# Kernel optimization log

Hardware: AMD Instinct MI355X
Metric: run time of the kernel (lower is better)

The kernel has to match this reference:

```python
import jax, jax.numpy as jnp
import numpy as np

LMDA = 1.0
SMOOTH = 1e-05

# 13 directional offsets (dz, dy, dx) matching the original slice pairs 1..13
OFFSETS = [
    (1, 0, 0), (0, 1, 0), (0, 0, 1),
    (1, 1, 0), (1, -1, 0),
    (0, 1, 1), (0, 1, -1),
    (1, 0, -1), (1, 0, 1),
    (1, -1, -1), (1, 1, -1),
    (-1, -1, -1), (-1, 1, -1),
]


def _shifted_diff(x, off):
    """x[..., pos-shift] - x[..., neg-shift] for offset off over last 3 dims."""
    sl_pos = tuple(slice(1, None) if o == 1 else (slice(None, -1) if o == -1 else slice(None)) for o in off)
    sl_neg = tuple(slice(None, -1) if o == 1 else (slice(1, None) if o == -1 else slice(None)) for o in off)
    return x[(Ellipsis,) + sl_pos] - x[(Ellipsis,) + sl_neg]


def setup_inputs() -> dict:
    key = jax.random.key(0)
    k1, k2 = jax.random.split(key)
    shape = (4, 1, 128, 192, 192)
    eps = 1e-6
    inp = jax.random.uniform(k1, shape, dtype=jnp.float32, minval=eps, maxval=1.0 - eps)
    tgt = jax.random.uniform(k2, shape, dtype=jnp.float32, minval=0.0, maxval=1.0)
    return {"input": inp, "target": tgt}


def reference(input, target):
    # region term: BCE with mean reduction
    bce = -jnp.mean(target * jnp.log(input) + (1.0 - target) * jnp.log(1.0 - input))

    # boundary term: 13 directional diff-product ratios
    acc = jnp.float32(0.0)
    for off in OFFSETS:
        di = _shifted_diff(input, off)
        dt = _shifted_diff(target, off)
        acc = acc + jnp.sum(di * dt) / (jnp.sum(dt * dt) + SMOOTH)
    boundary = 1.0 - acc / 13.0

    return LMDA * bce + boundary
```

## Files before the change

### kernel.cpp

```cpp
#include <hip/hip_runtime.h>
#include <math.h>

#define DX 192
#define DY 192
#define DZ 128
#define DB 4
#define DXY (DX*DY)
#define NTOT (DB*DZ*DXY)
#define NV (NTOT/4)
#define XV (DX/4)


__device__ inline float wred(float v) {
    #pragma unroll
    for (int o = 32; o > 0; o >>= 1) v += __shfl_down(v, o, 64);
    return v;
}

__global__ __launch_bounds__(256) void gc3d_main(const float* __restrict__ inp,
                                                 const float* __restrict__ tgt,
                                                 double* __restrict__ acc) {
    float s0=0,s1=0,s2=0,s3=0,s4=0,s5=0,s6=0,s7=0,s8=0,s9=0,s10=0,s11=0,s12=0;
    float r0=0,r1=0,r2=0,r3=0,r4=0,r5=0,r6=0,r7=0,r8=0,r9=0,r10=0,r11=0,r12=0;
    float bces = 0.f;

    int tid = blockIdx.x * blockDim.x + threadIdx.x;
    int stride = gridDim.x * blockDim.x;

    for (int v = tid; v < NV; v += stride) {
        int xv4 = v % XV;
        int rem = v / XV;
        int y = rem % DY;
        int z = (rem / DY) % DZ;
        int x0 = xv4 * 4;

        bool zv = (z != DZ - 1);
        bool yv = (y != DY - 1);
        int oz = zv ? DXY : 0;
        int oy = yv ? DX : 0;
        int xe = (x0 != DX - 4) ? 4 : 3;
        float fz = zv ? 1.f : 0.f;
        float fy = yv ? 1.f : 0.f;
        float fx3 = (x0 != DX - 4) ? 1.f : 0.f;

        long base = (long)v * 4;
        const float* ip = inp + base;
        const float* tp = tgt + base;

        float4 i00 = *(const float4*)(ip);
        float4 i01 = *(const float4*)(ip + oy);
        float4 i10 = *(const float4*)(ip + oz);
        float4 i11 = *(const float4*)(ip + oz + oy);
        float4 t00 = *(const float4*)(tp);
        float4 t01 = *(const float4*)(tp + oy);
        float4 t10 = *(const float4*)(tp + oz);
        float4 t11 = *(const float4*)(tp + oz + oy);
        float i00e = ip[xe],        i01e = ip[oy + xe];
        float i10e = ip[oz + xe],   i11e = ip[oz + oy + xe];
        float t00e = tp[xe],        t01e = tp[oy + xe];
        float t10e = tp[oz + xe],   t11e = tp[oz + oy + xe];

        #define PROC_ELEM(c0,c1,c2,c3,c4,c5,c6,c7, d0,d1,d2,d3,d4,d5,d6,d7, FX) do { \
            float fzy = fz*fy, fyx = fy*(FX), fzx = fz*(FX), fzyx = fzy*(FX); \
            float di, dt, dtm; \
            di=c4-c0; dt=d4-d0; dtm=fz  *dt; s0 +=di*dtm; r0 +=dt*dtm; \
            di=c2-c0; dt=d2-d0; dtm=fy  *dt; s1 +=di*dtm; r1 +=dt*dtm; \
            di=c1-c0; dt=d1-d0; dtm=(FX)*dt; s2 +=di*dtm; r2 +=dt*dtm; \
            di=c6-c0; dt=d6-d0; dtm=fzy *dt; s3 +=di*dtm; r3 +=dt*dtm; \
            di=c4-c2; dt=d4-d2; dtm=fzy *dt; s4 +=di*dtm; r4 +=dt*dtm; \
            di=c3-c0; dt=d3-d0; dtm=fyx *dt; s5 +=di*dtm; r5 +=dt*dtm; \
            di=c2-c1; dt=d2-d1; dtm=fyx *dt; s6 +=di*dtm; r6 +=dt*dtm; \
            di=c4-c1; dt=d4-d1; dtm=fzx *dt; s7 +=di*dtm; r7 +=dt*dtm; \
            di=c5-c0; dt=d5-d0; dtm=fzx *dt; s8 +=di*dtm; r8 +=dt*dtm; \
            di=c4-c3; dt=d4-d3; dtm=fzyx*dt; s9 +=di*dtm; r9 +=dt*dtm; \
            di=c6-c1; dt=d6-d1; dtm=fzyx*dt; s10+=di*dtm; r10+=dt*dtm; \
            di=c7-c0; dt=d7-d0; dtm=fzyx*dt; s11+=di*dtm; r11+=dt*dtm; \
            di=c5-c2; dt=d5-d2; dtm=fzyx*dt; s12+=di*dtm; r12+=dt*dtm; \
            bces += d0*__logf(c0) + (1.0f - d0)*__logf(1.0f - c0); \
        } while (0)

        PROC_ELEM(i00.x,i00.y,i01.x,i01.y,i10.x,i10.y,i11.x,i11.y,
                  t00.x,t00.y,t01.x,t01.y,t10.x,t10.y,t11.x,t11.y, 1.0f);
        PROC_ELEM(i00.y,i00.z,i01.y,i01.z,i10.y,i10.z,i11.y,i11.z,
                  t00.y,t00.z,t01.y,t01.z,t10.y,t10.z,t11.y,t11.z, 1.0f);
        PROC_ELEM(i00.z,i00.w,i01.z,i01.w,i10.z,i10.w,i11.z,i11.w,
                  t00.z,t00.w,t01.z,t01.w,t10.z,t10.w,t11.z,t11.w, 1.0f);
        PROC_ELEM(i00.w,i00e, i01.w,i01e, i10.w,i10e, i11.w,i11e,
                  t00.w,t00e, t01.w,t01e, t10.w,t10e, t11.w,t11e, fx3);
        #undef PROC_ELEM
    }

    float vals[27] = {s0,s1,s2,s3,s4,s5,s6,s7,s8,s9,s10,s11,s12,
                      r0,r1,r2,r3,r4,r5,r6,r7,r8,r9,r10,r11,r12, bces};
    #pragma unroll
    for (int k = 0; k < 27; k++) vals[k] = wred(vals[k]);

    __shared__ float red[4][27];
    int lane = threadIdx.x & 63;
    int wave = threadIdx.x >> 6;
    if (lane == 0) {
        #pragma unroll
        for (int k = 0; k < 27; k++) red[wave][k] = vals[k];
    }
    __syncthreads();
    if (threadIdx.x < 27) {
        float t = red[0][threadIdx.x] + red[1][threadIdx.x]
                + red[2][threadIdx.x] + red[3][threadIdx.x];
        atomicAdd(&acc[threadIdx.x], (double)t);
    }
}

__global__ void gc3d_final(const double* __restrict__ acc, float* __restrict__ out) {
    if (threadIdx.x == 0 && blockIdx.x == 0) {
        double s = 0.0;
        #pragma unroll
        for (int k = 0; k < 13; k++) s += acc[k] / (acc[13 + k] + 1e-5);
        double bce = -acc[26] / (double)NTOT;
        out[0] = (float)(bce + 1.0 - s / 13.0);
    }
}

extern "C" void kernel_launch(void* const* d_in, const int* in_sizes, int n_in,
                              void* d_out, int out_size, void* d_ws, size_t ws_size,
                              hipStream_t stream) {
    const float* inp = (const float*)d_in[0];
    const float* tgt = (const float*)d_in[1];
    double* acc = (double*)d_ws;

    hipMemsetAsync(d_ws, 0, 27 * sizeof(double), stream);
    gc3d_main<<<1536, 256, 0, stream>>>(inp, tgt, acc);
    gc3d_final<<<1, 64, 0, stream>>>(acc, (float*)d_out);
}
```

Measured before the change: 223.3 us.

## March each thread along y segments reusing previous row loads and specialising boundaries

```diff
diff --git a/kernel.cpp b/kernel.cpp
--- a/kernel.cpp
+++ b/kernel.cpp
@@ -7,8 +7,10 @@
 #define DB 4
 #define DXY (DX*DY)
 #define NTOT (DB*DZ*DXY)
-#define NV (NTOT/4)
 #define XV (DX/4)
+#define NCOL (DB*DZ*XV)
+#define SEG 12
+#define NSEG (DY/SEG)
 
 
 __device__ inline float wred(float v) {
@@ -17,90 +19,141 @@
     return v;
 }
 
+__device__ inline float4 ld4(const float* p) { return *(const float4*)p; }
+
+#define TN(k, A1, A0, D1, D0) do { float di_=(A1)-(A0); float dt_=(D1)-(D0); \
+    sk[k] += di_*dt_; rk[k] += dt_*dt_; } while(0)
+#define TM(k, A1, A0, D1, D0) do { float di_=(A1)-(A0); float dt_=(D1)-(D0); \
+    float dm_=fx3*dt_; sk[k] += di_*dm_; rk[k] += dt_*dm_; } while(0)
+#define BCEACC(A0, D0) do { bces += (D0)*__logf(A0) + (1.0f-(D0))*__logf(1.0f-(A0)); } while(0)
+
+
+#define ELEM_FULL(a0,a1,a2,a3,a4,a5,a6,a7, d0,d1,d2,d3,d4,d5,d6,d7) do { \
+    TN(0,a4,a0,d4,d0); TN(1,a2,a0,d2,d0); TN(2,a1,a0,d1,d0); TN(3,a6,a0,d6,d0); \
+    TN(4,a4,a2,d4,d2); TN(5,a3,a0,d3,d0); TN(6,a2,a1,d2,d1); TN(7,a4,a1,d4,d1); \
+    TN(8,a5,a0,d5,d0); TN(9,a4,a3,d4,d3); TN(10,a6,a1,d6,d1); TN(11,a7,a0,d7,d0); \
+    TN(12,a5,a2,d5,d2); BCEACC(a0,d0); } while(0)
+
+#define ELEM_FX(a0,a1,a2,a3,a4,a5,a6,a7, d0,d1,d2,d3,d4,d5,d6,d7) do { \
+    TN(0,a4,a0,d4,d0); TN(1,a2,a0,d2,d0); TM(2,a1,a0,d1,d0); TN(3,a6,a0,d6,d0); \
+    TN(4,a4,a2,d4,d2); TM(5,a3,a0,d3,d0); TM(6,a2,a1,d2,d1); TM(7,a4,a1,d4,d1); \
+    TM(8,a5,a0,d5,d0); TM(9,a4,a3,d4,d3); TM(10,a6,a1,d6,d1); TM(11,a7,a0,d7,d0); \
+    TM(12,a5,a2,d5,d2); BCEACC(a0,d0); } while(0)
+
+#define PEL_FULL(a0,a1,a4,a5, d0,d1,d4,d5) do { \
+    TN(0,a4,a0,d4,d0); TN(2,a1,a0,d1,d0); TN(7,a4,a1,d4,d1); TN(8,a5,a0,d5,d0); \
+    BCEACC(a0,d0); } while(0)
+#define PEL_FX(a0,a1,a4,a5, d0,d1,d4,d5) do { \
+    TN(0,a4,a0,d4,d0); TM(2,a1,a0,d1,d0); TM(7,a4,a1,d4,d1); TM(8,a5,a0,d5,d0); \
+    BCEACC(a0,d0); } while(0)
+
+#define ZEL_FULL(a0,a1,a2,a3, d0,d1,d2,d3) do { \
+    TN(1,a2,a0,d2,d0); TN(2,a1,a0,d1,d0); TN(5,a3,a0,d3,d0); TN(6,a2,a1,d2,d1); \
+    BCEACC(a0,d0); } while(0)
+#define ZEL_FX(a0,a1,a2,a3, d0,d1,d2,d3) do { \
+    TN(1,a2,a0,d2,d0); TM(2,a1,a0,d1,d0); TM(5,a3,a0,d3,d0); TM(6,a2,a1,d2,d1); \
+    BCEACC(a0,d0); } while(0)
+
+#define ZPEL_FULL(a0,a1, d0,d1) do { TN(2,a1,a0,d1,d0); BCEACC(a0,d0); } while(0)
+#define ZPEL_FX(a0,a1, d0,d1)   do { TM(2,a1,a0,d1,d0); BCEACC(a0,d0); } while(0)
+
 __global__ __launch_bounds__(256) void gc3d_main(const float* __restrict__ inp,
                                                  const float* __restrict__ tgt,
                                                  double* __restrict__ acc) {
-    float s0=0,s1=0,s2=0,s3=0,s4=0,s5=0,s6=0,s7=0,s8=0,s9=0,s10=0,s11=0,s12=0;
-    float r0=0,r1=0,r2=0,r3=0,r4=0,r5=0,r6=0,r7=0,r8=0,r9=0,r10=0,r11=0,r12=0;
+    float sk[13] = {0,0,0,0,0,0,0,0,0,0,0,0,0};
+    float rk[13] = {0,0,0,0,0,0,0,0,0,0,0,0,0};
     float bces = 0.f;
 
-    int tid = blockIdx.x * blockDim.x + threadIdx.x;
-    int stride = gridDim.x * blockDim.x;
+    int c   = blockIdx.x * 256 + threadIdx.x;
+    int s   = blockIdx.y;
+    int xv4 = c % XV;
+    int zb  = c / XV;
+    int z   = zb & (DZ - 1);
+    int y0  = s * SEG;
+    bool xlast = (xv4 == XV - 1);
+    int   xe   = xlast ? 3 : 4;
+    float fx3  = xlast ? 0.f : 1.f;
+    bool lastseg = (s == NSEG - 1);
+    int  nfull   = SEG - (lastseg ? 1 : 0);
 
-    for (int v = tid; v < NV; v += stride) {
-        int xv4 = v % XV;
-        int rem = v / XV;
-        int y = rem % DY;
-        int z = (rem / DY) % DZ;
-        int x0 = xv4 * 4;
+    int base = (zb * DY + y0) * DX + xv4 * 4;
+    const float* ip = inp + base;
+    const float* tp = tgt + base;
 
-        bool zv = (z != DZ - 1);
-        bool yv = (y != DY - 1);
-        int oz = zv ? DXY : 0;
-        int oy = yv ? DX : 0;
-        int xe = (x0 != DX - 4) ? 4 : 3;
-        float fz = zv ? 1.f : 0.f;
-        float fy = yv ? 1.f : 0.f;
-        float fx3 = (x0 != DX - 4) ? 1.f : 0.f;
+    if (z != DZ - 1) {
+        const float* ipz = ip + DXY;
+        const float* tpz = tp + DXY;
+        float4 i0 = ld4(ip),  i1 = ld4(ipz);
+        float4 t0 = ld4(tp),  t1 = ld4(tpz);
+        float i0e = ip[xe],  i1e = ipz[xe];
+        float t0e = tp[xe],  t1e = tpz[xe];
 
-        long base = (long)v * 4;
-        const float* ip = inp + base;
-        const float* tp = tgt + base;
+        for (int it = 0; it < nfull; ++it) {
+            ip += DX; ipz += DX; tp += DX; tpz += DX;
+            float4 j0 = ld4(ip),  j1 = ld4(ipz);
+            float4 u0 = ld4(tp),  u1 = ld4(tpz);
+            float j0e = ip[xe],  j1e = ipz[xe];
+            float u0e = tp[xe],  u1e = tpz[xe];
 
-        float4 i00 = *(const float4*)(ip);
-        float4 i01 = *(const float4*)(ip + oy);
-        float4 i10 = *(const float4*)(ip + oz);
-        float4 i11 = *(const float4*)(ip + oz + oy);
-        float4 t00 = *(const float4*)(tp);
-        float4 t01 = *(const float4*)(tp + oy);
-        float4 t10 = *(const float4*)(tp + oz);
-        float4 t11 = *(const float4*)(tp + oz + oy);
-        float i00e = ip[xe],        i01e = ip[oy + xe];
-        float i10e = ip[oz + xe],   i11e = ip[oz + oy + xe];
-        float t00e = tp[xe],        t01e = tp[oy + xe];
-        float t10e = tp[oz + xe],   t11e = tp[oz + oy + xe];
+            ELEM_FULL(i0.x,i0.y, j0.x,j0.y, i1.x,i1.y, j1.x,j1.y,
+                      t0.x,t0.y, u0.x,u0.y, t1.x,t1.y, u1.x,u1.y);
+            ELEM_FULL(i0.y,i0.z, j0.y,j0.z, i1.y,i1.z, j1.y,j1.z,
+                      t0.y,t0.z, u0.y,u0.z, t1.y,t1.z, u1.y,u1.z);
+            ELEM_FULL(i0.z,i0.w, j0.z,j0.w, i1.z,i1.w, j1.z,j1.w,
+                      t0.z,t0.w, u0.z,u0.w, t1.z,t1.w, u1.z,u1.w);
+            ELEM_FX  (i0.w,i0e,  j0.w,j0e,  i1.w,i1e,  j1.w,j1e,
+                      t0.w,t0e,  u0.w,u0e,  t1.w,t1e,  u1.w,u1e);
 
-        #define PROC_ELEM(c0,c1,c2,c3,c4,c5,c6,c7, d0,d1,d2,d3,d4,d5,d6,d7, FX) do { \
-            float fzy = fz*fy, fyx = fy*(FX), fzx = fz*(FX), fzyx = fzy*(FX); \
-            float di, dt, dtm; \
-            di=c4-c0; dt=d4-d0; dtm=fz  *dt; s0 +=di*dtm; r0 +=dt*dtm; \
-            di=c2-c0; dt=d2-d0; dtm=fy  *dt; s1 +=di*dtm; r1 +=dt*dtm; \
-            di=c1-c0; dt=d1-d0; dtm=(FX)*dt; s2 +=di*dtm; r2 +=dt*dtm; \
-            di=c6-c0; dt=d6-d0; dtm=fzy *dt; s3 +=di*dtm; r3 +=dt*dtm; \
-            di=c4-c2; dt=d4-d2; dtm=fzy *dt; s4 +=di*dtm; r4 +=dt*dtm; \
-            di=c3-c0; dt=d3-d0; dtm=fyx *dt; s5 +=di*dtm; r5 +=dt*dtm; \
-            di=c2-c1; dt=d2-d1; dtm=fyx *dt; s6 +=di*dtm; r6 +=dt*dtm; \
-            di=c4-c1; dt=d4-d1; dtm=fzx *dt; s7 +=di*dtm; r7 +=dt*dtm; \
-            di=c5-c0; dt=d5-d0; dtm=fzx *dt; s8 +=di*dtm; r8 +=dt*dtm; \
-            di=c4-c3; dt=d4-d3; dtm=fzyx*dt; s9 +=di*dtm; r9 +=dt*dtm; \
-            di=c6-c1; dt=d6-d1; dtm=fzyx*dt; s10+=di*dtm; r10+=dt*dtm; \
-            di=c7-c0; dt=d7-d0; dtm=fzyx*dt; s11+=di*dtm; r11+=dt*dtm; \
-            di=c5-c2; dt=d5-d2; dtm=fzyx*dt; s12+=di*dtm; r12+=dt*dtm; \
-            bces += d0*__logf(c0) + (1.0f - d0)*__logf(1.0f - c0); \
-        } while (0)
+            i0 = j0; i1 = j1; t0 = u0; t1 = u1;
+            i0e = j0e; i1e = j1e; t0e = u0e; t1e = u1e;
+        }
+        if (lastseg) {
+            PEL_FULL(i0.x,i0.y, i1.x,i1.y, t0.x,t0.y, t1.x,t1.y);
+            PEL_FULL(i0.y,i0.z, i1.y,i1.z, t0.y,t0.z, t1.y,t1.z);
+            PEL_FULL(i0.z,i0.w, i1.z,i1.w, t0.z,t0.w, t1.z,t1.w);
+            PEL_FX  (i0.w,i0e,  i1.w,i1e,  t0.w,t0e,  t1.w,t1e);
+        }
+    } else {
+        float4 i0 = ld4(ip);
+        float4 t0 = ld4(tp);
+        float i0e = ip[xe];
+        float t0e = tp[xe];
 
-        PROC_ELEM(i00.x,i00.y,i01.x,i01.y,i10.x,i10.y,i11.x,i11.y,
-                  t00.x,t00.y,t01.x,t01.y,t10.x,t10.y,t11.x,t11.y, 1.0f);
-        PROC_ELEM(i00.y,i00.z,i01.y,i01.z,i10.y,i10.z,i11.y,i11.z,
-                  t00.y,t00.z,t01.y,t01.z,t10.y,t10.z,t11.y,t11.z, 1.0f);
-        PROC_ELEM(i00.z,i00.w,i01.z,i01.w,i10.z,i10.w,i11.z,i11.w,
-                  t00.z,t00.w,t01.z,t01.w,t10.z,t10.w,t11.z,t11.w, 1.0f);
-        PROC_ELEM(i00.w,i00e, i01.w,i01e, i10.w,i10e, i11.w,i11e,
-                  t00.w,t00e, t01.w,t01e, t10.w,t10e, t11.w,t11e, fx3);
-        #undef PROC_ELEM
+        for (int it = 0; it < nfull; ++it) {
+            ip += DX; tp += DX;
+            float4 j0 = ld4(ip);
+            float4 u0 = ld4(tp);
+            float j0e = ip[xe];
+            float u0e = tp[xe];
+
+            ZEL_FULL(i0.x,i0.y, j0.x,j0.y, t0.x,t0.y, u0.x,u0.y);
+            ZEL_FULL(i0.y,i0.z, j0.y,j0.z, t0.y,t0.z, u0.y,u0.z);
+            ZEL_FULL(i0.z,i0.w, j0.z,j0.w, t0.z,t0.w, u0.z,u0.w);
+            ZEL_FX  (i0.w,i0e,  j0.w,j0e,  t0.w,t0e,  u0.w,u0e);
+
+            i0 = j0; t0 = u0; i0e = j0e; t0e = u0e;
+        }
+        if (lastseg) {
+            ZPEL_FULL(i0.x,i0.y, t0.x,t0.y);
+            ZPEL_FULL(i0.y,i0.z, t0.y,t0.z);
+            ZPEL_FULL(i0.z,i0.w, t0.z,t0.w);
+            ZPEL_FX  (i0.w,i0e,  t0.w,t0e);
+        }
     }
 
-    float vals[27] = {s0,s1,s2,s3,s4,s5,s6,s7,s8,s9,s10,s11,s12,
-                      r0,r1,r2,r3,r4,r5,r6,r7,r8,r9,r10,r11,r12, bces};
+    float vals[27];
     #pragma unroll
-    for (int k = 0; k < 27; k++) vals[k] = wred(vals[k]);
+    for (int q = 0; q < 13; q++) { vals[q] = sk[q]; vals[13 + q] = rk[q]; }
+    vals[26] = bces;
+    #pragma unroll
+    for (int q = 0; q < 27; q++) vals[q] = wred(vals[q]);
 
     __shared__ float red[4][27];
     int lane = threadIdx.x & 63;
     int wave = threadIdx.x >> 6;
     if (lane == 0) {
         #pragma unroll
-        for (int k = 0; k < 27; k++) red[wave][k] = vals[k];
+        for (int q = 0; q < 27; q++) red[wave][q] = vals[q];
     }
     __syncthreads();
     if (threadIdx.x < 27) {
@@ -128,6 +181,7 @@
     double* acc = (double*)d_ws;
 
     hipMemsetAsync(d_ws, 0, 27 * sizeof(double), stream);
-    gc3d_main<<<1536, 256, 0, stream>>>(inp, tgt, acc);
+    dim3 grid(NCOL / 256, NSEG);
+    gc3d_main<<<grid, 256, 0, stream>>>(inp, tgt, acc);
     gc3d_final<<<1, 64, 0, stream>>>(acc, (float*)d_out);
 }
```

Measured after the change: 231.5 us. 3.7% more time.
